# Kernel tuning notes

Hardware: AMD Instinct MI355X
Metric: run time of the kernel (lower is better)

## Reference

```python
import jax, jax.numpy as jnp
import numpy as np

H = 64

def _lstm_cell(x, h, c, Wih, Whh, bih, bhh):
    # x: [B, in], h/c: [B, H]; gate order i, f, g, o (PyTorch convention)
    g = x @ Wih.T + h @ Whh.T + (bih + bhh)
    i, f, gg, o = jnp.split(g, 4, axis=-1)
    i = jax.nn.sigmoid(i)
    f = jax.nn.sigmoid(f)
    gg = jnp.tanh(gg)
    o = jax.nn.sigmoid(o)
    c_new = f * c + i * gg
    h_new = o * jnp.tanh(c_new)
    return h_new, c_new


def setup_inputs() -> dict:
    key = jax.random.key(0)
    ks = jax.random.split(key, 12)
    B, T = 512, 1024
    s1 = 1.0 / np.sqrt(H)
    u = lambda k, shape: jax.random.uniform(k, shape, jnp.float32, -s1, s1)
    return {
        "x": jax.random.normal(ks[0], (B, T), jnp.float32),
        "W_ih1": u(ks[1], (4 * H, 1)),
        "W_hh1": u(ks[2], (4 * H, H)),
        "b_ih1": u(ks[3], (4 * H,)),
        "b_hh1": u(ks[4], (4 * H,)),
        "W_ih2": u(ks[5], (4 * H, H)),
        "W_hh2": u(ks[6], (4 * H, H)),
        "b_ih2": u(ks[7], (4 * H,)),
        "b_hh2": u(ks[8], (4 * H,)),
        "W_l": u(ks[9], (1, H)),
        "b_l": u(ks[10], (1,)),
        "future": 64,
    }


def reference(x, W_ih1, W_hh1, b_ih1, b_hh1, W_ih2, W_hh2, b_ih2, b_hh2, W_l, b_l, future):
    B, T = x.shape
    h1 = jnp.zeros((B, H), jnp.float32)
    c1 = jnp.zeros((B, H), jnp.float32)
    h2 = jnp.zeros((B, H), jnp.float32)
    c2 = jnp.zeros((B, H), jnp.float32)

    def step(carry, xt):
        h1, c1, h2, c2 = carry
        h1, c1 = _lstm_cell(xt, h1, c1, W_ih1, W_hh1, b_ih1, b_hh1)
        h2, c2 = _lstm_cell(h1, h2, c2, W_ih2, W_hh2, b_ih2, b_hh2)
        out = h2 @ W_l.T + b_l  # [B, 1]
        return (h1, c1, h2, c2), out

    xs = x.T[:, :, None]  # [T, B, 1]
    (h1, c1, h2, c2), outs = jax.lax.scan(step, (h1, c1, h2, c2), xs)
    last_out = outs[-1]  # [B, 1]

    def fstep(carry, _):
        h1, c1, h2, c2, out = carry
        h1, c1 = _lstm_cell(out, h1, c1, W_ih1, W_hh1, b_ih1, b_hh1)
        h2, c2 = _lstm_cell(h1, h2, c2, W_ih2, W_hh2, b_ih2, b_hh2)
        out = h2 @ W_l.T + b_l
        return (h1, c1, h2, c2, out), out

    if future > 0:
        _, fouts = jax.lax.scan(fstep, (h1, c1, h2, c2, last_out), None, length=future)
        outs = jnp.concatenate([outs, fouts], axis=0)  # [T+future, B, 1]

    return outs[:, :, 0].T  # [B, T+future]
```

## Files before the change

kernel.cpp:

```cpp
#include <hip/hip_runtime.h>

#define TMAIN 1024
#define TFUT  64
#define TTOT  (TMAIN + TFUT)

__device__ __forceinline__ float sig_(float x) {
    return 1.0f / (1.0f + __expf(-x));
}
__device__ __forceinline__ float tanh_(float x) {
    x = fminf(15.0f, fmaxf(-15.0f, x));
    float e = __expf(-2.0f * x);
    return (1.0f - e) / (1.0f + e);
}

__global__ __launch_bounds__(256, 2)
void lstm2_kernel(const float* __restrict__ x,
                  const float* __restrict__ Wih1,
                  const float* __restrict__ Whh1,
                  const float* __restrict__ bih1,
                  const float* __restrict__ bhh1,
                  const float* __restrict__ Wih2,
                  const float* __restrict__ Whh2,
                  const float* __restrict__ bih2,
                  const float* __restrict__ bhh2,
                  const float* __restrict__ Wl,
                  const float* __restrict__ bl,
                  float* __restrict__ out)
{
    const int b    = blockIdx.x;
    const int tid  = threadIdx.x;
    const int wv   = tid >> 6;
    const int lane = tid & 63;
    const int q    = lane >> 4;
    const int unit = (wv << 4) + (lane & 15);
    const int row  = (q << 6) + unit;

    float4 w1[16], w2a[16], w2b[16];
    const float4* W1r  = reinterpret_cast<const float4*>(Whh1 + row * 64);
    const float4* W2ar = reinterpret_cast<const float4*>(Wih2 + row * 64);
    const float4* W2br = reinterpret_cast<const float4*>(Whh2 + row * 64);
#pragma unroll
    for (int j = 0; j < 16; ++j) { w1[j] = W1r[j]; w2a[j] = W2ar[j]; w2b[j] = W2br[j]; }

    const float wih1r = Wih1[row];
    const float bias1 = bih1[row] + bhh1[row];
    const float bias2 = bih2[row] + bhh2[row];
    const float wlu   = Wl[unit];
    const float bl0   = bl[0];

    __shared__ __align__(16) float h1buf[2][64];
    __shared__ __align__(16) float h2buf[2][64];
    __shared__ __align__(16) float psum[4];

    if (tid < 64) {
        h1buf[0][tid] = 0.0f; h1buf[1][tid] = 0.0f;
        h2buf[0][tid] = 0.0f; h2buf[1][tid] = 0.0f;
    }
    __syncthreads();

    float c1 = 0.0f, c2 = 0.0f, xv = 0.0f;
    const float* xb = x + b * TMAIN;
    float* ob = out + b * TTOT;

    for (int s = 0; s < TTOT; ++s) {
        const int p = s & 1;
        const float x_t = (s < TMAIN) ? xb[s] : xv;

        float acc = fmaf(wih1r, x_t, bias1);
        const float4* h1o = reinterpret_cast<const float4*>(h1buf[p]);
#pragma unroll
        for (int j = 0; j < 16; ++j) {
            float4 h = h1o[j];
            acc = fmaf(w1[j].x, h.x, acc);
            acc = fmaf(w1[j].y, h.y, acc);
            acc = fmaf(w1[j].z, h.z, acc);
            acc = fmaf(w1[j].w, h.w, acc);
        }
        float gv = (q == 2) ? tanh_(acc) : sig_(acc);
        float v1 = __shfl_xor(gv, 16, 64);
        float v2 = __shfl_xor(gv, 32, 64);
        float v3 = __shfl_xor(v1, 32, 64);
        float gi = (q == 0) ? gv : (q == 1) ? v1 : (q == 2) ? v2 : v3;
        float gf = (q == 1) ? gv : (q == 0) ? v1 : (q == 3) ? v2 : v3;
        float gg = (q == 2) ? gv : (q == 3) ? v1 : (q == 0) ? v2 : v3;
        float go = (q == 3) ? gv : (q == 2) ? v1 : (q == 1) ? v2 : v3;
        c1 = fmaf(gf, c1, gi * gg);
        const float h1n = go * tanh_(c1);
        if (q == 0) h1buf[p ^ 1][unit] = h1n;
        __syncthreads();

        acc = bias2;
        const float4* h1v = reinterpret_cast<const float4*>(h1buf[p ^ 1]);
        const float4* h2o = reinterpret_cast<const float4*>(h2buf[p]);
#pragma unroll
        for (int j = 0; j < 16; ++j) {
            float4 h = h1v[j];
            acc = fmaf(w2a[j].x, h.x, acc);
            acc = fmaf(w2a[j].y, h.y, acc);
            acc = fmaf(w2a[j].z, h.z, acc);
            acc = fmaf(w2a[j].w, h.w, acc);
        }
#pragma unroll
        for (int j = 0; j < 16; ++j) {
            float4 h = h2o[j];
            acc = fmaf(w2b[j].x, h.x, acc);
            acc = fmaf(w2b[j].y, h.y, acc);
            acc = fmaf(w2b[j].z, h.z, acc);
            acc = fmaf(w2b[j].w, h.w, acc);
        }
        gv = (q == 2) ? tanh_(acc) : sig_(acc);
        v1 = __shfl_xor(gv, 16, 64);
        v2 = __shfl_xor(gv, 32, 64);
        v3 = __shfl_xor(v1, 32, 64);
        gi = (q == 0) ? gv : (q == 1) ? v1 : (q == 2) ? v2 : v3;
        gf = (q == 1) ? gv : (q == 0) ? v1 : (q == 3) ? v2 : v3;
        gg = (q == 2) ? gv : (q == 3) ? v1 : (q == 0) ? v2 : v3;
        go = (q == 3) ? gv : (q == 2) ? v1 : (q == 1) ? v2 : v3;
        c2 = fmaf(gf, c2, gi * gg);
        const float h2n = go * tanh_(c2);
        if (q == 0) h2buf[p ^ 1][unit] = h2n;

        float pv = (q == 0) ? wlu * h2n : 0.0f;
#pragma unroll
        for (int m = 1; m < 64; m <<= 1) pv += __shfl_xor(pv, m, 64);
        if (lane == 0) psum[wv] = pv;
        __syncthreads();

        const float4 ps = *reinterpret_cast<const float4*>(psum);
        xv = ps.x + ps.y + ps.z + ps.w + bl0;
        if (tid == 0) ob[s] = xv;
    }
}

extern "C" void kernel_launch(void* const* d_in, const int* in_sizes, int n_in,
                              void* d_out, int out_size, void* d_ws, size_t ws_size,
                              hipStream_t stream)
{
    const float* xx   = (const float*)d_in[0];
    const float* Wih1 = (const float*)d_in[1];
    const float* Whh1 = (const float*)d_in[2];
    const float* bih1 = (const float*)d_in[3];
    const float* bhh1 = (const float*)d_in[4];
    const float* Wih2 = (const float*)d_in[5];
    const float* Whh2 = (const float*)d_in[6];
    const float* bih2 = (const float*)d_in[7];
    const float* bhh2 = (const float*)d_in[8];
    const float* Wl   = (const float*)d_in[9];
    const float* bl   = (const float*)d_in[10];
    float* out = (float*)d_out;

    lstm2_kernel<<<dim3(512), dim3(256), 0, stream>>>(
        xx, Wih1, Whh1, bih1, bhh1, Wih2, Whh2, bih2, bhh2, Wl, bl, out);
}
```

Before: 1.994 ms.

## Broadcast hidden state via readlane from registers instead of LDS float4 reads

Each lane now holds one hidden-state element in a register, and the matvec broadcasts operands with v_readlane into scalar registers, so the inner loops no longer issue LDS loads. The activation code is unified into a single exp-based sigmoid form shared by tanh and sigmoid, and the dot products are split over four accumulators to shorten dependency chains. The output projection is done by every wave redundantly from the broadcast h2, removing the psum shared buffer and the double buffering. The cost is 192 readlane instructions per step, which have scalar-pipe latency, and higher register pressure from the flattened weight arrays.

```diff
diff --git a/kernel.cpp b/kernel.cpp
--- a/kernel.cpp
+++ b/kernel.cpp
@@ -4,13 +4,8 @@
 #define TFUT  64
 #define TTOT  (TMAIN + TFUT)
 
-__device__ __forceinline__ float sig_(float x) {
-    return 1.0f / (1.0f + __expf(-x));
-}
-__device__ __forceinline__ float tanh_(float x) {
-    x = fminf(15.0f, fmaxf(-15.0f, x));
-    float e = __expf(-2.0f * x);
-    return (1.0f - e) / (1.0f + e);
+__device__ __forceinline__ float rl_(float v, int k) {
+    return __uint_as_float(__builtin_amdgcn_readlane(__float_as_uint(v), k));
 }
 
 __global__ __launch_bounds__(256, 2)
@@ -35,100 +30,115 @@
     const int unit = (wv << 4) + (lane & 15);
     const int row  = (q << 6) + unit;
 
-    float4 w1[16], w2a[16], w2b[16];
-    const float4* W1r  = reinterpret_cast<const float4*>(Whh1 + row * 64);
-    const float4* W2ar = reinterpret_cast<const float4*>(Wih2 + row * 64);
-    const float4* W2br = reinterpret_cast<const float4*>(Whh2 + row * 64);
+    float w1f[64], w2af[64], w2bf[64];
+    {
+        const float4* p1 = reinterpret_cast<const float4*>(Whh1 + row * 64);
+        const float4* p2 = reinterpret_cast<const float4*>(Wih2 + row * 64);
+        const float4* p3 = reinterpret_cast<const float4*>(Whh2 + row * 64);
 #pragma unroll
-    for (int j = 0; j < 16; ++j) { w1[j] = W1r[j]; w2a[j] = W2ar[j]; w2b[j] = W2br[j]; }
+        for (int j = 0; j < 16; ++j) {
+            float4 a = p1[j];
+            float4 c = p2[j];
+            float4 d = p3[j];
+            asm volatile("" : "+v"(a.x), "+v"(a.y), "+v"(a.z), "+v"(a.w));
+            asm volatile("" : "+v"(c.x), "+v"(c.y), "+v"(c.z), "+v"(c.w));
+            asm volatile("" : "+v"(d.x), "+v"(d.y), "+v"(d.z), "+v"(d.w));
+            w1f[4*j+0]=a.x; w1f[4*j+1]=a.y; w1f[4*j+2]=a.z; w1f[4*j+3]=a.w;
+            w2af[4*j+0]=c.x; w2af[4*j+1]=c.y; w2af[4*j+2]=c.z; w2af[4*j+3]=c.w;
+            w2bf[4*j+0]=d.x; w2bf[4*j+1]=d.y; w2bf[4*j+2]=d.z; w2bf[4*j+3]=d.w;
+        }
+    }
 
     const float wih1r = Wih1[row];
     const float bias1 = bih1[row] + bhh1[row];
     const float bias2 = bih2[row] + bhh2[row];
-    const float wlu   = Wl[unit];
+    const float wl_l  = Wl[lane];
     const float bl0   = bl[0];
 
-    __shared__ __align__(16) float h1buf[2][64];
-    __shared__ __align__(16) float h2buf[2][64];
-    __shared__ __align__(16) float psum[4];
+    __shared__ __align__(16) float h1buf[64];
+    __shared__ __align__(16) float h2buf[64];
 
-    if (tid < 64) {
-        h1buf[0][tid] = 0.0f; h1buf[1][tid] = 0.0f;
-        h2buf[0][tid] = 0.0f; h2buf[1][tid] = 0.0f;
-    }
-    __syncthreads();
+    float vh1o = 0.0f, vh2o = 0.0f;
+    float c1 = 0.0f, c2 = 0.0f, xv = 0.0f;
 
-    float c1 = 0.0f, c2 = 0.0f, xv = 0.0f;
     const float* xb = x + b * TMAIN;
     float* ob = out + b * TTOT;
 
     for (int s = 0; s < TTOT; ++s) {
-        const int p = s & 1;
         const float x_t = (s < TMAIN) ? xb[s] : xv;
 
-        float acc = fmaf(wih1r, x_t, bias1);
-        const float4* h1o = reinterpret_cast<const float4*>(h1buf[p]);
+        float a0 = 0.f, a1 = 0.f, a2 = 0.f, a3 = 0.f;
 #pragma unroll
-        for (int j = 0; j < 16; ++j) {
-            float4 h = h1o[j];
-            acc = fmaf(w1[j].x, h.x, acc);
-            acc = fmaf(w1[j].y, h.y, acc);
-            acc = fmaf(w1[j].z, h.z, acc);
-            acc = fmaf(w1[j].w, h.w, acc);
+        for (int k = 0; k < 64; k += 4) {
+            a0 = fmaf(rl_(vh1o, k+0), w1f[k+0], a0);
+            a1 = fmaf(rl_(vh1o, k+1), w1f[k+1], a1);
+            a2 = fmaf(rl_(vh1o, k+2), w1f[k+2], a2);
+            a3 = fmaf(rl_(vh1o, k+3), w1f[k+3], a3);
         }
-        float gv = (q == 2) ? tanh_(acc) : sig_(acc);
-        float v1 = __shfl_xor(gv, 16, 64);
-        float v2 = __shfl_xor(gv, 32, 64);
-        float v3 = __shfl_xor(v1, 32, 64);
-        float gi = (q == 0) ? gv : (q == 1) ? v1 : (q == 2) ? v2 : v3;
-        float gf = (q == 1) ? gv : (q == 0) ? v1 : (q == 3) ? v2 : v3;
-        float gg = (q == 2) ? gv : (q == 3) ? v1 : (q == 0) ? v2 : v3;
-        float go = (q == 3) ? gv : (q == 2) ? v1 : (q == 1) ? v2 : v3;
-        c1 = fmaf(gf, c1, gi * gg);
-        const float h1n = go * tanh_(c1);
-        if (q == 0) h1buf[p ^ 1][unit] = h1n;
+        float acc = fmaf(wih1r, x_t, bias1) + ((a0 + a1) + (a2 + a3));
+
+        {
+            float earg = (q == 2) ? -2.0f * acc : -acc;
+            float r = 1.0f / (1.0f + __expf(earg));
+            float gv = (q == 2) ? 2.0f * r - 1.0f : r;
+            float v1 = __shfl_xor(gv, 16, 64);
+            float v2 = __shfl_xor(gv, 32, 64);
+            float v3 = __shfl_xor(v1, 32, 64);
+            float gi = (q == 0) ? gv : (q == 1) ? v1 : (q == 2) ? v2 : v3;
+            float gf = (q == 1) ? gv : (q == 0) ? v1 : (q == 3) ? v2 : v3;
+            float gg = (q == 2) ? gv : (q == 3) ? v1 : (q == 0) ? v2 : v3;
+            float go = (q == 3) ? gv : (q == 2) ? v1 : (q == 1) ? v2 : v3;
+            c1 = fmaf(gf, c1, gi * gg);
+            float tr = 1.0f / (1.0f + __expf(-2.0f * c1));
+            float h1n = go * (2.0f * tr - 1.0f);
+            if (q == 0) h1buf[unit] = h1n;
+        }
         __syncthreads();
+        const float vh1n = h1buf[lane];
 
-        acc = bias2;
-        const float4* h1v = reinterpret_cast<const float4*>(h1buf[p ^ 1]);
-        const float4* h2o = reinterpret_cast<const float4*>(h2buf[p]);
+        a0 = 0.f; a1 = 0.f; a2 = 0.f; a3 = 0.f;
 #pragma unroll
-        for (int j = 0; j < 16; ++j) {
-            float4 h = h1v[j];
-            acc = fmaf(w2a[j].x, h.x, acc);
-            acc = fmaf(w2a[j].y, h.y, acc);
-            acc = fmaf(w2a[j].z, h.z, acc);
-            acc = fmaf(w2a[j].w, h.w, acc);
+        for (int k = 0; k < 64; k += 4) {
+            a0 = fmaf(rl_(vh1n, k+0), w2af[k+0], a0);
+            a1 = fmaf(rl_(vh1n, k+1), w2af[k+1], a1);
+            a2 = fmaf(rl_(vh1n, k+2), w2af[k+2], a2);
+            a3 = fmaf(rl_(vh1n, k+3), w2af[k+3], a3);
         }
 #pragma unroll
-        for (int j = 0; j < 16; ++j) {
-            float4 h = h2o[j];
-            acc = fmaf(w2b[j].x, h.x, acc);
-            acc = fmaf(w2b[j].y, h.y, acc);
-            acc = fmaf(w2b[j].z, h.z, acc);
-            acc = fmaf(w2b[j].w, h.w, acc);
+        for (int k = 0; k < 64; k += 4) {
+            a0 = fmaf(rl_(vh2o, k+0), w2bf[k+0], a0);
+            a1 = fmaf(rl_(vh2o, k+1), w2bf[k+1], a1);
+            a2 = fmaf(rl_(vh2o, k+2), w2bf[k+2], a2);
+            a3 = fmaf(rl_(vh2o, k+3), w2bf[k+3], a3);
         }
-        gv = (q == 2) ? tanh_(acc) : sig_(acc);
-        v1 = __shfl_xor(gv, 16, 64);
-        v2 = __shfl_xor(gv, 32, 64);
-        v3 = __shfl_xor(v1, 32, 64);
-        gi = (q == 0) ? gv : (q == 1) ? v1 : (q == 2) ? v2 : v3;
-        gf = (q == 1) ? gv : (q == 0) ? v1 : (q == 3) ? v2 : v3;
-        gg = (q == 2) ? gv : (q == 3) ? v1 : (q == 0) ? v2 : v3;
-        go = (q == 3) ? gv : (q == 2) ? v1 : (q == 1) ? v2 : v3;
-        c2 = fmaf(gf, c2, gi * gg);
-        const float h2n = go * tanh_(c2);
-        if (q == 0) h2buf[p ^ 1][unit] = h2n;
+        acc = bias2 + ((a0 + a1) + (a2 + a3));
+        {
+            float earg = (q == 2) ? -2.0f * acc : -acc;
+            float r = 1.0f / (1.0f + __expf(earg));
+            float gv = (q == 2) ? 2.0f * r - 1.0f : r;
+            float v1 = __shfl_xor(gv, 16, 64);
+            float v2 = __shfl_xor(gv, 32, 64);
+            float v3 = __shfl_xor(v1, 32, 64);
+            float gi = (q == 0) ? gv : (q == 1) ? v1 : (q == 2) ? v2 : v3;
+            float gf = (q == 1) ? gv : (q == 0) ? v1 : (q == 3) ? v2 : v3;
+            float gg = (q == 2) ? gv : (q == 3) ? v1 : (q == 0) ? v2 : v3;
+            float go = (q == 3) ? gv : (q == 2) ? v1 : (q == 1) ? v2 : v3;
+            c2 = fmaf(gf, c2, gi * gg);
+            float tr = 1.0f / (1.0f + __expf(-2.0f * c2));
+            float h2n = go * (2.0f * tr - 1.0f);
+            if (q == 0) h2buf[unit] = h2n;
+        }
+        __syncthreads();
+        const float vh2n = h2buf[lane];
 
-        float pv = (q == 0) ? wlu * h2n : 0.0f;
+        float pv = wl_l * vh2n;
 #pragma unroll
         for (int m = 1; m < 64; m <<= 1) pv += __shfl_xor(pv, m, 64);
-        if (lane == 0) psum[wv] = pv;
-        __syncthreads();
+        xv = pv + bl0;
+        if (tid == 0) ob[s] = xv;
 
-        const float4 ps = *reinterpret_cast<const float4*>(psum);
-        xv = ps.x + ps.y + ps.z + ps.w + bl0;
-        if (tid == 0) ob[s] = xv;
+        vh1o = vh1n;
+        vh2o = vh2n;
     }
 }
 
```

Measured after the change: 2.518 ms. +26.3%, slower.
